# Performance work log

Measured on AMD Instinct MI355X. Metric: run time of the kernel, lower is better.

Reference implementation:

```python
import jax, jax.numpy as jnp
import numpy as np

D_STATE = 16
D_CONV = 4


def _ln_cf(x, w, b, eps=1e-6):
    # channels_first LayerNorm over dim 1 of (B,C,H,W)
    u = x.mean(1, keepdims=True)
    s = ((x - u) ** 2).mean(1, keepdims=True)
    return w[:, None, None] * ((x - u) / jnp.sqrt(s + eps)) + b[:, None, None]


def _ln_last(x, w, b, eps=1e-5):
    u = x.mean(-1, keepdims=True)
    s = ((x - u) ** 2).mean(-1, keepdims=True)
    return (x - u) / jnp.sqrt(s + eps) * w + b


def _mamba(xn, Win, convw, convb, Wx, Wdt, bdt, Alog, Dp):
    # xn: (B, L, d_model); returns (B, L, d_inner) (out_proj is Identity in this module)
    B, L, _ = xn.shape
    di = Win.shape[0] // 2
    xz = xn @ Win.T                                   # (B,L,2*di), in_proj bias=False
    xc, z = xz[..., :di], xz[..., di:]
    # causal depthwise conv1d along L (pad left d_conv-1, slice == torch pad+trim)
    xt = jnp.pad(xc.transpose(0, 2, 1), ((0, 0), (0, 0), (D_CONV - 1, 0)))
    xt = jax.lax.conv_general_dilated(xt, convw[:, None, :], (1,), 'VALID',
                                      dimension_numbers=('NCH', 'OIH', 'NCH'),
                                      feature_group_count=di)
    xs = jax.nn.silu(xt + convb[None, :, None]).transpose(0, 2, 1)  # (B,L,di)
    dtr = Wdt.shape[1]
    x_dbl = xs @ Wx.T                                 # (B,L,dtr+2*ds)
    dt = x_dbl[..., :dtr]
    Bm = x_dbl[..., dtr:dtr + D_STATE]                # (B,L,ds)
    Cm = x_dbl[..., dtr + D_STATE:]                   # (B,L,ds)
    delta = jax.nn.softplus(dt @ Wdt.T + bdt)         # (B,L,di)
    A = -jnp.exp(Alog)                                # (di,ds)
    dA = jnp.exp(delta[..., None] * A)                # (B,L,di,ds)
    dBx = delta[..., None] * Bm[:, :, None, :] * xs[..., None]

    def step(h, ab):
        a, b2 = ab
        h = a * h + b2
        return h, h

    h0 = jnp.zeros((B, di, D_STATE), xn.dtype)
    _, hs = jax.lax.scan(step, h0, (dA.transpose(1, 0, 2, 3), dBx.transpose(1, 0, 2, 3)))
    y = jnp.einsum('lbds,bls->bld', hs, Cm) + xs * Dp
    return y * jax.nn.silu(z)


def _dwconv2d(u, k, dil):
    c = k.shape[0]
    return jax.lax.conv_general_dilated(u, k[:, None], (1, 1),
                                        [(dil, dil), (dil, dil)],
                                        rhs_dilation=(dil, dil),
                                        dimension_numbers=('NCHW', 'OIHW', 'NCHW'),
                                        feature_group_count=c)


def _block(x, gamma1, gamma2, ln1_w, ln1_b, mn_w, mn_b,
           f_Win, f_convw, f_convb, f_Wx, f_Wdt, f_bdt, f_Alog, f_D,
           b_Win, b_convw, b_convb, b_Wx, b_Wdt, b_bdt, b_Alog, b_D,
           Wout, msff_win, msff_dw1, msff_dw2, msff_dw3, msff_wout):
    B, C, H, W = x.shape
    L = H * W
    # --- BiPixelMambaLayer branch ---
    x1 = _ln_cf(x, ln1_w, ln1_b)                       # norm1 (channels_first)
    xf = x1.reshape(B, C, L).transpose(0, 2, 1)        # (B,L,C)
    xn = _ln_last(xf, mn_w, mn_b)                      # inner nn.LayerNorm (eps=1e-5)
    yf = _mamba(xn, f_Win, f_convw, f_convb, f_Wx, f_Wdt, f_bdt, f_Alog, f_D)
    yb = _mamba(xn[:, ::-1], b_Win, b_convw, b_convb, b_Wx, b_Wdt, b_bdt, b_Alog, b_D)
    yo = (yf + yb[:, ::-1]) @ Wout.T                   # shared out_proj (bias=False)
    x = x + gamma1[:, None, None] * (yo.transpose(0, 2, 1).reshape(B, C, H, W) + x1)
    # --- MSFF branch (norm1 reused) ---
    inp = x
    xm = _ln_cf(x, ln1_w, ln1_b)
    h = jnp.einsum('oc,bchw->bohw', msff_win, xm)      # project_in (1x1x1 conv, depth=1)
    hid = msff_dw1.shape[0]
    h1 = _dwconv2d(h[:, :hid], msff_dw1, 1)            # Conv3d 3x3x3 w/ depth=1 == 2D center slice
    h2 = _dwconv2d(h[:, hid:2 * hid], msff_dw2, 2)
    h3 = _dwconv2d(h[:, 2 * hid:], msff_dw3, 3)
    g = jax.nn.gelu(h1, approximate=False) * h2 * h3
    xm = jnp.einsum('oc,bchw->bohw', msff_wout, g)     # project_out
    return inp + gamma2[:, None, None] * xm


def setup_inputs() -> dict:
    key = jax.random.key(0)
    ks = jax.random.split(key, 40)
    dim, di, dtr, ds, hid, Bn, H, W = 96, 192, 6, 16, 192, 2, 64, 64
    r = lambda i, shape, s=0.05: jax.random.normal(ks[i], shape, jnp.float32) * s
    inp = {
        'x': r(0, (Bn, dim, H, W), 1.0),
        'gamma1': r(1, (dim,), 0.1), 'gamma2': r(2, (dim,), 0.1),
        'ln1_w': 1.0 + r(3, (dim,), 0.1), 'ln1_b': r(4, (dim,), 0.1),
        'mn_w': 1.0 + r(5, (dim,), 0.1), 'mn_b': r(6, (dim,), 0.1),
    }
    i = 7
    for p in ('f_', 'b_'):
        inp[p + 'Win'] = r(i, (2 * di, dim)); i += 1
        inp[p + 'convw'] = r(i, (di, D_CONV), 0.2); i += 1
        inp[p + 'convb'] = r(i, (di,), 0.1); i += 1
        inp[p + 'Wx'] = r(i, (dtr + 2 * ds, di)); i += 1
        inp[p + 'Wdt'] = r(i, (di, dtr), 0.1); i += 1
        inp[p + 'bdt'] = r(i, (di,), 0.1); i += 1
        inp[p + 'Alog'] = jax.random.uniform(ks[i], (di, ds), jnp.float32, 0.0, 2.5); i += 1
        inp[p + 'D'] = r(i, (di,), 0.5); i += 1
    inp['Wout'] = r(i, (dim, di)); i += 1
    inp['msff_win'] = r(i, (3 * hid, dim)); i += 1
    inp['msff_dw1'] = r(i, (hid, 3, 3), 0.2); i += 1
    inp['msff_dw2'] = r(i, (hid, 3, 3), 0.2); i += 1
    inp['msff_dw3'] = r(i, (hid, 3, 3), 0.2); i += 1
    inp['msff_wout'] = r(i, (dim, hid)); i += 1
    return inp


def reference(x, gamma1, gamma2, ln1_w, ln1_b, mn_w, mn_b,
              f_Win, f_convw, f_convb, f_Wx, f_Wdt, f_bdt, f_Alog, f_D,
              b_Win, b_convw, b_convb, b_Wx, b_Wdt, b_bdt, b_Alog, b_D,
              Wout, msff_win, msff_dw1, msff_dw2, msff_dw3, msff_wout):
    return _block(x, gamma1, gamma2, ln1_w, ln1_b, mn_w, mn_b,
                  f_Win, f_convw, f_convb, f_Wx, f_Wdt, f_bdt, f_Alog, f_D,
                  b_Win, b_convw, b_convb, b_Wx, b_Wdt, b_bdt, b_Alog, b_D,
                  Wout, msff_win, msff_dw1, msff_dw2, msff_dw3, msff_wout)
```

## Files before the change

### kernel.cpp

```cpp
#include <hip/hip_runtime.h>
#include <hip/hip_bf16.h>
#include <math.h>

typedef __hip_bfloat16 bf16;
typedef _Float16 f16;
typedef f16  f16x8  __attribute__((ext_vector_type(8)));
typedef short short8 __attribute__((ext_vector_type(8)));
typedef float floatx4 __attribute__((ext_vector_type(4)));

#define L_SEQ 4096
#define BATCH 2
#define DIM   96
#define DI    192
#define DS    16
#define HID   192
#define NPOS  (BATCH * L_SEQ)
#define NCH   512
#define CHUNK 8
#define NREC  (2 * BATCH * DI)
#define LDBL  40
#define LOG2E 1.44269504088896f
#define TP    32

__device__ __forceinline__ float silu_f(float x) { return x / (1.f + __expf(-x)); }
__device__ __forceinline__ float softplus_f(float x) {
    return fmaxf(x, 0.f) + __logf(1.f + __expf(-fabsf(x)));
}
__device__ __forceinline__ float b2f(bf16 v) { return __bfloat162float(v); }

__global__ void k_cast_w(const float* __restrict__ fWin, const float* __restrict__ bWin,
                         const float* __restrict__ fWx,  const float* __restrict__ bWx,
                         const float* __restrict__ Wout, const float* __restrict__ mwin,
                         const float* __restrict__ mwout, bf16* __restrict__ arena) {
    int i = blockIdx.x * blockDim.x + threadIdx.x;
    if (i >= 180480) return;
    float v;
    if (i < 36864)        v = fWin[i];
    else if (i < 73728)   v = bWin[i - 36864];
    else if (i < 81024)   v = fWx[i - 73728];
    else if (i < 88320)   v = bWx[i - 81024];
    else if (i < 106752)  v = Wout[i - 88320];
    else if (i < 162048)  v = mwin[i - 106752];
    else                  v = mwout[i - 162048];
    arena[i] = __float2bfloat16(v);
}

__global__ void k_ln12_t(const float* __restrict__ x,
                         const float* __restrict__ ln1w, const float* __restrict__ ln1b,
                         const float* __restrict__ mnw,  const float* __restrict__ mnb,
                         float* __restrict__ X1, bf16* __restrict__ XNbf) {
    __shared__ float xt[DIM][TP + 1];
    __shared__ float rs[8][TP], rss[8][TP];
    __shared__ float uu[TP], rr[TP];
    int p0 = blockIdx.x * TP;
    int b = p0 >> 12, l0 = p0 & (L_SEQ - 1);
    int t = threadIdx.x;
    int tg = t >> 5, li = t & 31;

    for (int idx = t; idx < DIM * TP; idx += 256) {
        int c = idx >> 5, q = idx & 31;
        xt[c][q] = x[((size_t)(b * DIM + c)) * L_SEQ + l0 + q];
    }
    __syncthreads();
    {
        float s = 0.f, ss = 0.f;
        for (int c = tg; c < DIM; c += 8) { float v = xt[c][li]; s += v; ss += v * v; }
        rs[tg][li] = s; rss[tg][li] = ss;
    }
    __syncthreads();
    if (t < TP) {
        float s = 0.f, ss = 0.f;
#pragma unroll
        for (int g = 0; g < 8; g++) { s += rs[g][t]; ss += rss[g][t]; }
        float u = s / DIM;
        uu[t] = u; rr[t] = rsqrtf(ss / DIM - u * u + 1e-6f);
    }
    __syncthreads();
    {
        float u = uu[li], r = rr[li];
        float s2 = 0.f, ss2 = 0.f;
        for (int c = tg; c < DIM; c += 8) {
            float tv = ln1w[c] * (xt[c][li] - u) * r + ln1b[c];
            X1[((size_t)(b * DIM + c)) * L_SEQ + l0 + li] = tv;
            xt[c][li] = tv;
            s2 += tv; ss2 += tv * tv;
        }
        rs[tg][li] = s2; rss[tg][li] = ss2;
    }
    __syncthreads();
    if (t < TP) {
        float s = 0.f, ss = 0.f;
#pragma unroll
        for (int g = 0; g < 8; g++) { s += rs[g][t]; ss += rss[g][t]; }
        float u = s / DIM;
        uu[t] = u; rr[t] = rsqrtf(ss / DIM - u * u + 1e-5f);
    }
    __syncthreads();
    for (int idx = t; idx < DIM * TP; idx += 256) {
        int q = idx / DIM, c = idx % DIM;
        XNbf[(size_t)(p0 + q) * DIM + c] =
            __float2bfloat16((xt[c][q] - uu[q]) * rr[q] * mnw[c] + mnb[c]);
    }
}

__global__ void mfma_nt_dir(const bf16* __restrict__ A0, const bf16* __restrict__ A1,
                            const bf16* __restrict__ W0, const bf16* __restrict__ W1,
                            void* __restrict__ C0, void* __restrict__ C1,
                            int M, int N, int K, int ldc, int pad6, int obf) {
    int z = blockIdx.z;
    const bf16* A = z ? A1 : A0;
    const bf16* W = z ? W1 : W0;
    void* C = z ? C1 : C0;
    int wave = threadIdx.x >> 6, lane = threadIdx.x & 63;
    int m0 = blockIdx.x * 64 + wave * 16;
    int n0 = blockIdx.y * 64;
    int lm = lane & 15, quad = lane >> 4;
    const short* Ap = (const short*)A + (size_t)(m0 + lm) * K + quad * 8;
    const short* Wp = (const short*)W;
    floatx4 acc[4];
#pragma unroll
    for (int t = 0; t < 4; t++) acc[t] = (floatx4){0.f, 0.f, 0.f, 0.f};
    for (int k0 = 0; k0 < K; k0 += 32) {
        short8 a = *(const short8*)(Ap + k0);
#pragma unroll
        for (int t = 0; t < 4; t++) {
            int n = n0 + t * 16 + lm;
            short8 b = (n < N) ? *(const short8*)(Wp + (size_t)n * K + k0 + quad * 8)
                               : (short8){0,0,0,0,0,0,0,0};
            acc[t] = __builtin_amdgcn_mfma_f32_16x16x32_bf16(a, b, acc[t], 0, 0, 0);
        }
    }
#pragma unroll
    for (int t = 0; t < 4; t++) {
        int n = n0 + t * 16 + lm;
        if (n < N) {
            int nn = (pad6 && n >= 6) ? n + 2 : n;
#pragma unroll
            for (int r = 0; r < 4; r++) {
                int m = m0 + quad * 4 + r;
                if (obf) ((bf16*)C)[(size_t)m * ldc + nn] = __float2bfloat16(acc[t][r]);
                else     ((float*)C)[(size_t)m * ldc + nn] = acc[t][r];
            }
        }
    }
}

__global__ void mfma_nt(const bf16* __restrict__ A, const bf16* __restrict__ W,
                        bf16* __restrict__ C, int M, int N, int K, int ldc) {
    int wave = threadIdx.x >> 6, lane = threadIdx.x & 63;
    int m0 = blockIdx.x * 64 + wave * 16;
    int n0 = blockIdx.y * 64;
    int lm = lane & 15, quad = lane >> 4;
    const short* Ap = (const short*)A + (size_t)(m0 + lm) * K + quad * 8;
    const short* Wp = (const short*)W;
    floatx4 acc[4];
#pragma unroll
    for (int t = 0; t < 4; t++) acc[t] = (floatx4){0.f, 0.f, 0.f, 0.f};
    for (int k0 = 0; k0 < K; k0 += 32) {
        short8 a = *(const short8*)(Ap + k0);
#pragma unroll
        for (int t = 0; t < 4; t++) {
            int n = n0 + t * 16 + lm;
            short8 b = (n < N) ? *(const short8*)(Wp + (size_t)n * K + k0 + quad * 8)
                               : (short8){0,0,0,0,0,0,0,0};
            acc[t] = __builtin_amdgcn_mfma_f32_16x16x32_bf16(a, b, acc[t], 0, 0, 0);
        }
    }
#pragma unroll
    for (int t = 0; t < 4; t++) {
        int n = n0 + t * 16 + lm;
        if (n < N) {
#pragma unroll
            for (int r = 0; r < 4; r++) {
                int m = m0 + quad * 4 + r;
                C[(size_t)m * ldc + n] = __float2bfloat16(acc[t][r]);
            }
        }
    }
}

__global__ void mfma_out(const bf16* __restrict__ Y1, const bf16* __restrict__ Y2,
                         const bf16* __restrict__ W, float* __restrict__ C,
                         int M, int N, int K, int ldc) {
    int wave = threadIdx.x >> 6, lane = threadIdx.x & 63;
    int m0 = blockIdx.x * 64 + wave * 16;
    int n0 = blockIdx.y * 64;
    int lm = lane & 15, quad = lane >> 4;
    const short* A1p = (const short*)Y1 + (size_t)(m0 + lm) * K + quad * 8;
    const short* A2p = (const short*)Y2 + (size_t)(m0 + lm) * K + quad * 8;
    const short* Wp  = (const short*)W;
    floatx4 acc[4];
#pragma unroll
    for (int t = 0; t < 4; t++) acc[t] = (floatx4){0.f, 0.f, 0.f, 0.f};
    for (int k0 = 0; k0 < K; k0 += 32) {
        short8 a1 = *(const short8*)(A1p + k0);
        short8 a2 = *(const short8*)(A2p + k0);
#pragma unroll
        for (int t = 0; t < 4; t++) {
            int n = n0 + t * 16 + lm;
            short8 b = (n < N) ? *(const short8*)(Wp + (size_t)n * K + k0 + quad * 8)
                               : (short8){0,0,0,0,0,0,0,0};
            acc[t] = __builtin_amdgcn_mfma_f32_16x16x32_bf16(a1, b, acc[t], 0, 0, 0);
            acc[t] = __builtin_amdgcn_mfma_f32_16x16x32_bf16(a2, b, acc[t], 0, 0, 0);
        }
    }
#pragma unroll
    for (int t = 0; t < 4; t++) {
        int n = n0 + t * 16 + lm;
        if (n < N) {
#pragma unroll
            for (int r = 0; r < 4; r++) {
                int m = m0 + quad * 4 + r;
                C[(size_t)m * ldc + n] = acc[t][r];
            }
        }
    }
}

__global__ void mfma_msffout(const bf16* __restrict__ A, const bf16* __restrict__ Bm,
                             const float* __restrict__ XMID, const float* __restrict__ gamma2,
                             float* __restrict__ out, int M, int K) {
    int wave = threadIdx.x >> 6, lane = threadIdx.x & 63;
    int m0 = blockIdx.x * 64 + wave * 16;
    int n0 = blockIdx.y * 64;
    int lm = lane & 15, quad = lane >> 4;
    int am = m0 + lm;
    bool aval = am < M;
    const short* Ap = (const short*)A + (size_t)am * K + quad * 8;
    const short* Bp = (const short*)Bm;
    floatx4 acc[4];
#pragma unroll
    for (int t = 0; t < 4; t++) acc[t] = (floatx4){0.f, 0.f, 0.f, 0.f};
    for (int k0 = 0; k0 < K; k0 += 32) {
        short8 a = aval ? *(const short8*)(Ap + k0) : (short8){0,0,0,0,0,0,0,0};
#pragma unroll
        for (int t = 0; t < 4; t++) {
            int n = n0 + t * 16 + lm;
            short8 b = *(const short8*)(Bp + (size_t)n * K + k0 + quad * 8);
            acc[t] = __builtin_amdgcn_mfma_f32_16x16x32_bf16(a, b, acc[t], 0, 0, 0);
        }
    }
#pragma unroll
    for (int t = 0; t < 4; t++) {
        int n = n0 + t * 16 + lm;
        int b = n >> 12, l = n & (L_SEQ - 1);
#pragma unroll
        for (int r = 0; r < 4; r++) {
            int m = m0 + quad * 4 + r;
            if (m < M) {
                size_t idx = ((size_t)(b * M + m)) * L_SEQ + l;
                out[idx] = XMID[idx] + gamma2[m] * acc[t][r];
            }
        }
    }
}

__global__ void k_conv(const bf16* __restrict__ XZF, const bf16* __restrict__ XZB,
                       const float* __restrict__ fw, const float* __restrict__ fb,
                       const float* __restrict__ bw, const float* __restrict__ bb,
                       bf16* __restrict__ XSF, bf16* __restrict__ XSB) {
    int dirb = blockIdx.y;
    int i = blockIdx.x * blockDim.x + threadIdx.x;
    int d = i % DI;
    int p = i / DI;
    int b = p >> 12, l = p & (L_SEQ - 1);
    const bf16* XZ = dirb ? XZB : XZF;
    const float* cw = dirb ? bw : fw;
    float acc = (dirb ? bb : fb)[d];
    if (!dirb) {
#pragma unroll
        for (int k = 0; k < 4; k++) {
            int ls = l - 3 + k;
            if (ls >= 0) acc += cw[d * 4 + k] * b2f(XZ[((size_t)(b * L_SEQ + ls)) * 384 + d]);
        }
    } else {
#pragma unroll
        for (int k = 0; k < 4; k++) {
            int ls = l + 3 - k;
            if (ls < L_SEQ) acc += cw[d * 4 + k] * b2f(XZ[((size_t)(b * L_SEQ + ls)) * 384 + d]);
        }
    }
    (dirb ? XSB : XSF)[(size_t)p * DI + d] = __float2bfloat16(silu_f(acc));
}

__global__ void k_scan_p1(const float* __restrict__ DBLF, const float* __restrict__ DBLB,
                          const bf16* __restrict__ XSF,  const bf16* __restrict__ XSB,
                          const float* __restrict__ fWdt, const float* __restrict__ fbdt,
                          const float* __restrict__ bWdt, const float* __restrict__ bbdt,
                          const float* __restrict__ fAlog, const float* __restrict__ bAlog,
                          f16* __restrict__ P, f16* __restrict__ Q) {
    int t = blockIdx.x * blockDim.x + threadIdx.x;
    int d = t % DI;
    int g = t / DI;
    int chunk = g & (NCH - 1);
    int dirb = g >> 9;
    int b = dirb & 1, dir = dirb >> 1;

    const float* DBL = dir ? DBLB : DBLF;
    const bf16*  XS  = dir ? XSB  : XSF;
    const float* al  = (dir ? bAlog : fAlog) + d * DS;
    const float* wdt = (dir ? bWdt : fWdt) + d * 6;
    float bdtv = (dir ? bbdt : fbdt)[d];

    float wd[6];
#pragma unroll
    for (int r = 0; r < 6; r++) wd[r] = wdt[r];
    float A2[16], h[16];
#pragma unroll
    for (int s = 0; s < 16; s++) { A2[s] = -__expf(al[s]) * LOG2E; h[s] = 0.f; }

    int l = dir ? (L_SEQ - 1 - chunk * CHUNK) : chunk * CHUNK;
    int stp = dir ? -1 : 1;
    float sumdel = 0.f;

    for (int i = 0; i < CHUNK; i++) {
        size_t p = (size_t)b * L_SEQ + l;
        const float* row = DBL + p * LDBL;
        float dtv = bdtv;
#pragma unroll
        for (int r = 0; r < 6; r++) dtv += row[r] * wd[r];
        float del = softplus_f(dtv);
        float xs  = b2f(XS[p * DI + d]);
        const float4* bm = (const float4*)(row + 8);
        float4 B0 = bm[0], B1 = bm[1], B2 = bm[2], B3 = bm[3];
        float Bm[16] = {B0.x,B0.y,B0.z,B0.w, B1.x,B1.y,B1.z,B1.w,
                        B2.x,B2.y,B2.z,B2.w, B3.x,B3.y,B3.z,B3.w};
        float dx = del * xs;
        sumdel += del;
#pragma unroll
        for (int s = 0; s < 16; s++) {
            float dA = exp2f(del * A2[s]);
            h[s] = dA * h[s] + dx * Bm[s];
        }
        l += stp;
    }
    size_t idx = ((size_t)g * DI + d) * 16;
    f16x8 q0, q1, p0, p1;
#pragma unroll
    for (int j = 0; j < 8; j++) {
        q0[j] = (f16)h[j];
        q1[j] = (f16)h[8 + j];
        p0[j] = (f16)exp2f(A2[j] * sumdel);
        p1[j] = (f16)exp2f(A2[8 + j] * sumdel);
    }
    *(f16x8*)(Q + idx)     = q0;
    *(f16x8*)(Q + idx + 8) = q1;
    *(f16x8*)(P + idx)     = p0;
    *(f16x8*)(P + idx + 8) = p1;
}

__global__ void k_scan_p2(const f16* __restrict__ P, f16* __restrict__ Q) {
    int u = blockIdx.x * blockDim.x + threadIdx.x;
    int s = u & 15;
    int dd = (u >> 4) % DI;
    int dirb = u / (DI * 16);
    float run = 0.f;
#pragma unroll 8
    for (int c = 0; c < NCH; c++) {
        size_t i = (((size_t)(dirb * NCH + c)) * DI + dd) * 16 + s;
        float tmp = (float)Q[i];
        Q[i] = (f16)run;
        run = (float)P[i] * run + tmp;
    }
}

__global__ void k_scan_p3(const float* __restrict__ DBLF, const float* __restrict__ DBLB,
                          const bf16* __restrict__ XSF,  const bf16* __restrict__ XSB,
                          const bf16* __restrict__ XZF,  const bf16* __restrict__ XZB,
                          const float* __restrict__ fWdt, const float* __restrict__ fbdt,
                          const float* __restrict__ bWdt, const float* __restrict__ bbdt,
                          const float* __restrict__ fAlog, const float* __restrict__ bAlog,
                          const float* __restrict__ fD,    const float* __restrict__ bD,
                          const f16* __restrict__ Q,
                          bf16* __restrict__ YSF, bf16* __restrict__ YSB) {
    int t = blockIdx.x * blockDim.x + threadIdx.x;
    int d = t % DI;
    int g = t / DI;
    int chunk = g & (NCH - 1);
    int dirb = g >> 9;
    int b = dirb & 1, dir = dirb >> 1;

    const float* DBL = dir ? DBLB : DBLF;
    const bf16*  XS  = dir ? XSB  : XSF;
    const bf16*  XZ  = dir ? XZB  : XZF;
    const float* al  = (dir ? bAlog : fAlog) + d * DS;
    const float* wdt = (dir ? bWdt : fWdt) + d * 6;
    float bdtv = (dir ? bbdt : fbdt)[d];
    float Dp = dir ? bD[d] : fD[d];
    bf16* Y = dir ? YSB : YSF;

    float wd[6];
#pragma unroll
    for (int r = 0; r < 6; r++) wd[r] = wdt[r];
    float A2[16], h[16];
#pragma unroll
    for (int s = 0; s < 16; s++) A2[s] = -__expf(al[s]) * LOG2E;
    size_t idx = ((size_t)g * DI + d) * 16;
    f16x8 q0 = *(const f16x8*)(Q + idx);
    f16x8 q1 = *(const f16x8*)(Q + idx + 8);
#pragma unroll
    for (int j = 0; j < 8; j++) { h[j] = (float)q0[j]; h[8 + j] = (float)q1[j]; }

    int l = dir ? (L_SEQ - 1 - chunk * CHUNK) : chunk * CHUNK;
    int stp = dir ? -1 : 1;

    for (int i = 0; i < CHUNK; i++) {
        size_t p = (size_t)b * L_SEQ + l;
        const float* row = DBL + p * LDBL;
        float dtv = bdtv;
#pragma unroll
        for (int r = 0; r < 6; r++) dtv += row[r] * wd[r];
        float del = softplus_f(dtv);
        float xs  = b2f(XS[p * DI + d]);
        float z   = b2f(XZ[p * 384 + 192 + d]);
        const float4* bm = (const float4*)(row + 8);
        float4 B0 = bm[0], B1 = bm[1], B2 = bm[2], B3 = bm[3];
        float4 C0 = bm[4], C1 = bm[5], C2 = bm[6], C3 = bm[7];
        float Bm[16] = {B0.x,B0.y,B0.z,B0.w, B1.x,B1.y,B1.z,B1.w,
                        B2.x,B2.y,B2.z,B2.w, B3.x,B3.y,B3.z,B3.w};
        float Cm[16] = {C0.x,C0.y,C0.z,C0.w, C1.x,C1.y,C1.z,C1.w,
                        C2.x,C2.y,C2.z,C2.w, C3.x,C3.y,C3.z,C3.w};
        float dx = del * xs;
        float pr = 0.f;
#pragma unroll
        for (int s = 0; s < 16; s++) {
            float dA = exp2f(del * A2[s]);
            h[s] = dA * h[s] + dx * Bm[s];
            pr += h[s] * Cm[s];
        }
        Y[p * DI + d] = __float2bfloat16((pr + xs * Dp) * silu_f(z));
        l += stp;
    }
}

__global__ void k_mid_t(const float* __restrict__ x, const float* __restrict__ YO,
                        const float* __restrict__ X1,
                        const float* __restrict__ gamma1,
                        const float* __restrict__ ln1w, const float* __restrict__ ln1b,
                        float* __restrict__ XMID, bf16* __restrict__ XM2cl) {
    __shared__ float vt[DIM][TP + 1];
    __shared__ float yt[DIM][TP + 1];
    __shared__ float rs[8][TP], rss[8][TP];
    __shared__ float uu[TP], rr[TP];
    int p0 = blockIdx.x * TP;
    int b = p0 >> 12, l0 = p0 & (L_SEQ - 1);
    int t = threadIdx.x;
    int tg = t >> 5, li = t & 31;

    for (int idx = t; idx < DIM * TP; idx += 256) {
        int q = idx / DIM, c = idx % DIM;
        yt[c][q] = YO[(size_t)(p0 + q) * DIM + c];
    }
    __syncthreads();
    {
        float s = 0.f, ss = 0.f;
        for (int c = tg; c < DIM; c += 8) {
            size_t gi = ((size_t)(b * DIM + c)) * L_SEQ + l0 + li;
            float v = x[gi] + gamma1[c] * (yt[c][li] + X1[gi]);
            XMID[gi] = v;
            vt[c][li] = v;
            s += v; ss += v * v;
        }
        rs[tg][li] = s; rss[tg][li] = ss;
    }
    __syncthreads();
    if (t < TP) {
        float s = 0.f, ss = 0.f;
#pragma unroll
        for (int g = 0; g < 8; g++) { s += rs[g][t]; ss += rss[g][t]; }
        float u = s / DIM;
        uu[t] = u; rr[t] = rsqrtf(ss / DIM - u * u + 1e-6f);
    }
    __syncthreads();
    for (int idx = t; idx < DIM * TP; idx += 256) {
        int q = idx / DIM, c = idx % DIM;
        XM2cl[(size_t)(p0 + q) * DIM + c] =
            __float2bfloat16(ln1w[c] * (vt[c][q] - uu[q]) * rr[q] + ln1b[c]);
    }
}

__global__ void k_msff(const bf16* __restrict__ H,
                       const float* __restrict__ dw1, const float* __restrict__ dw2,
                       const float* __restrict__ dw3, bf16* __restrict__ G) {
    int i = blockIdx.x * blockDim.x + threadIdx.x;
    int c = i % HID;
    int p = i / HID;
    int b = p >> 12, l = p & (L_SEQ - 1);
    int y = l >> 6, xc = l & 63;
    float a1 = 0.f, a2 = 0.f, a3 = 0.f;
#pragma unroll
    for (int ky = 0; ky < 3; ky++) {
#pragma unroll
        for (int kx = 0; kx < 3; kx++) {
            float w1 = dw1[(c * 3 + ky) * 3 + kx];
            float w2 = dw2[(c * 3 + ky) * 3 + kx];
            float w3 = dw3[(c * 3 + ky) * 3 + kx];
            int y1 = y + (ky - 1), x1 = xc + (kx - 1);
            if (y1 >= 0 && y1 < 64 && x1 >= 0 && x1 < 64)
                a1 += w1 * b2f(H[((size_t)(b * L_SEQ + y1 * 64 + x1)) * 576 + c]);
            int y2 = y + (ky - 1) * 2, x2 = xc + (kx - 1) * 2;
            if (y2 >= 0 && y2 < 64 && x2 >= 0 && x2 < 64)
                a2 += w2 * b2f(H[((size_t)(b * L_SEQ + y2 * 64 + x2)) * 576 + 192 + c]);
            int y3 = y + (ky - 1) * 3, x3 = xc + (kx - 1) * 3;
            if (y3 >= 0 && y3 < 64 && x3 >= 0 && x3 < 64)
                a3 += w3 * b2f(H[((size_t)(b * L_SEQ + y3 * 64 + x3)) * 576 + 384 + c]);
        }
    }
    float ge = 0.5f * a1 * (1.f + erff(a1 * 0.70710678118f));
    G[(size_t)p * HID + c] = __float2bfloat16(ge * a2 * a3);
}

extern "C" void kernel_launch(void* const* d_in, const int* in_sizes, int n_in,
                              void* d_out, int out_size, void* d_ws, size_t ws_size,
                              hipStream_t stream) {
    const float* x      = (const float*)d_in[0];
    const float* gamma1 = (const float*)d_in[1];
    const float* gamma2 = (const float*)d_in[2];
    const float* ln1w   = (const float*)d_in[3];
    const float* ln1b   = (const float*)d_in[4];
    const float* mnw    = (const float*)d_in[5];
    const float* mnb    = (const float*)d_in[6];
    const float* fWin   = (const float*)d_in[7];
    const float* fconvw = (const float*)d_in[8];
    const float* fconvb = (const float*)d_in[9];
    const float* fWx    = (const float*)d_in[10];
    const float* fWdt   = (const float*)d_in[11];
    const float* fbdt   = (const float*)d_in[12];
    const float* fAlog  = (const float*)d_in[13];
    const float* fD     = (const float*)d_in[14];
    const float* bWin   = (const float*)d_in[15];
    const float* bconvw = (const float*)d_in[16];
    const float* bconvb = (const float*)d_in[17];
    const float* bWx    = (const float*)d_in[18];
    const float* bWdt   = (const float*)d_in[19];
    const float* bbdt   = (const float*)d_in[20];
    const float* bAlog  = (const float*)d_in[21];
    const float* bD     = (const float*)d_in[22];
    const float* Wout   = (const float*)d_in[23];
    const float* mwin   = (const float*)d_in[24];
    const float* mdw1   = (const float*)d_in[25];
    const float* mdw2   = (const float*)d_in[26];
    const float* mdw3   = (const float*)d_in[27];
    const float* mwout  = (const float*)d_in[28];
    float* out = (float*)d_out;

    float* ws = (float*)d_ws;
    float* R0    = ws;
    float* X1    = ws + 786432;
    float* XZFr  = ws + 1572864;
    float* XZBr  = ws + 3145728;
    float* XSr   = ws + 4718592;
    float* DBLF  = ws + 6291456;
    float* DBLB  = ws + 6619136;
    float* YSr   = ws + 6946816;
    float* Qr    = ws + 10092544;
    bf16*  WAR   = (bf16*)(ws + 13238272);

    bf16*  XNbf  = (bf16*)R0;
    float* YO    = R0;
    bf16*  XZF   = (bf16*)XZFr;
    bf16*  XZB   = (bf16*)XZBr;
    bf16*  XSF   = (bf16*)XSr;
    bf16*  XSB   = XSF + 1572864;
    f16*   Qh    = (f16*)Qr;
    f16*   Ph    = (f16*)YSr;
    bf16*  YSFbf = (bf16*)YSr;
    bf16*  YSBbf = YSFbf + 1572864;
    float* XMID  = Qr;
    bf16*  XM2cl = (bf16*)(Qr + 786432);
    bf16*  Hcl   = (bf16*)XZFr;
    bf16*  Gcl   = (bf16*)YSr;

    const bf16* fWinB  = WAR;
    const bf16* bWinB  = WAR + 36864;
    const bf16* fWxB   = WAR + 73728;
    const bf16* bWxB   = WAR + 81024;
    const bf16* WoutB  = WAR + 88320;
    const bf16* mwinB  = WAR + 106752;
    const bf16* mwoutB = WAR + 162048;

    k_cast_w<<<705, 256, 0, stream>>>(fWin, bWin, fWx, bWx, Wout, mwin, mwout, WAR);
    k_ln12_t<<<NPOS / TP, 256, 0, stream>>>(x, ln1w, ln1b, mnw, mnb, X1, XNbf);
    mfma_nt_dir<<<dim3(128, 6, 2), 256, 0, stream>>>(XNbf, XNbf, fWinB, bWinB,
                                                     XZF, XZB, NPOS, 384, DIM, 384, 0, 1);
    k_conv<<<dim3(NPOS * DI / 256, 2), 256, 0, stream>>>(XZF, XZB, fconvw, fconvb,
                                                         bconvw, bconvb, XSF, XSB);
    mfma_nt_dir<<<dim3(128, 1, 2), 256, 0, stream>>>(XSF, XSB, fWxB, bWxB,
                                                     DBLF, DBLB, NPOS, 38, DI, LDBL, 1, 0);
    k_scan_p1<<<NREC * NCH / 256, 256, 0, stream>>>(DBLF, DBLB, XSF, XSB,
                                                    fWdt, fbdt, bWdt, bbdt,
                                                    fAlog, bAlog, Ph, Qh);
    k_scan_p2<<<NREC * 16 / 256, 256, 0, stream>>>(Ph, Qh);
    k_scan_p3<<<NREC * NCH / 256, 256, 0, stream>>>(DBLF, DBLB, XSF, XSB, XZF, XZB,
                                                    fWdt, fbdt, bWdt, bbdt,
                                                    fAlog, bAlog, fD, bD, Qh,
                                                    YSFbf, YSBbf);
    mfma_out<<<dim3(128, 2), 256, 0, stream>>>(YSFbf, YSBbf, WoutB, YO, NPOS, DIM, DI, DIM);
    k_mid_t<<<NPOS / TP, 256, 0, stream>>>(x, YO, X1, gamma1, ln1w, ln1b, XMID, XM2cl);
    mfma_nt<<<dim3(128, 9), 256, 0, stream>>>(XM2cl, mwinB, Hcl, NPOS, 576, DIM, 576);
    k_msff<<<NPOS * HID / 256, 256, 0, stream>>>(Hcl, mdw1, mdw2, mdw3, Gcl);
    mfma_msffout<<<dim3(2, 128), 256, 0, stream>>>(mwoutB, Gcl, XMID, gamma2, out, DIM, HID);
}
```

Measured before the change: 316.1 us.

## Vectorize conv and MSFF kernels, precompute scan tables, halve scan chunk size

```diff
diff --git a/kernel.cpp b/kernel.cpp
--- a/kernel.cpp
+++ b/kernel.cpp
@@ -6,6 +6,7 @@
 typedef _Float16 f16;
 typedef f16  f16x8  __attribute__((ext_vector_type(8)));
 typedef short short8 __attribute__((ext_vector_type(8)));
+typedef unsigned short ushort8 __attribute__((ext_vector_type(8)));
 typedef float floatx4 __attribute__((ext_vector_type(4)));
 
 #define L_SEQ 4096
@@ -15,8 +16,8 @@
 #define DS    16
 #define HID   192
 #define NPOS  (BATCH * L_SEQ)
-#define NCH   512
-#define CHUNK 8
+#define NCH   1024
+#define CHUNK 4
 #define NREC  (2 * BATCH * DI)
 #define LDBL  40
 #define LOG2E 1.44269504088896f
@@ -27,22 +28,42 @@
     return fmaxf(x, 0.f) + __logf(1.f + __expf(-fabsf(x)));
 }
 __device__ __forceinline__ float b2f(bf16 v) { return __bfloat162float(v); }
-
-__global__ void k_cast_w(const float* __restrict__ fWin, const float* __restrict__ bWin,
-                         const float* __restrict__ fWx,  const float* __restrict__ bWx,
-                         const float* __restrict__ Wout, const float* __restrict__ mwin,
-                         const float* __restrict__ mwout, bf16* __restrict__ arena) {
+__device__ __forceinline__ float us2f(unsigned short u) {
+    union { unsigned int i; float f; } cv; cv.i = ((unsigned int)u) << 16; return cv.f;
+}
+
+__global__ void k_prep(const float* __restrict__ fWin, const float* __restrict__ bWin,
+                       const float* __restrict__ fWx,  const float* __restrict__ bWx,
+                       const float* __restrict__ Wout, const float* __restrict__ mwin,
+                       const float* __restrict__ mwout,
+                       const float* __restrict__ fAlog, const float* __restrict__ bAlog,
+                       const float* __restrict__ mdw1, const float* __restrict__ mdw2,
+                       const float* __restrict__ mdw3,
+                       bf16* __restrict__ war, float* __restrict__ a2tab,
+                       float* __restrict__ mdwt) {
     int i = blockIdx.x * blockDim.x + threadIdx.x;
-    if (i >= 180480) return;
-    float v;
-    if (i < 36864)        v = fWin[i];
-    else if (i < 73728)   v = bWin[i - 36864];
-    else if (i < 81024)   v = fWx[i - 73728];
-    else if (i < 88320)   v = bWx[i - 81024];
-    else if (i < 106752)  v = Wout[i - 88320];
-    else if (i < 162048)  v = mwin[i - 106752];
-    else                  v = mwout[i - 162048];
-    arena[i] = __float2bfloat16(v);
+    if (i < 180480) {
+        float v;
+        if (i < 36864)        v = fWin[i];
+        else if (i < 73728)   v = bWin[i - 36864];
+        else if (i < 81024)   v = fWx[i - 73728];
+        else if (i < 88320)   v = bWx[i - 81024];
+        else if (i < 106752)  v = Wout[i - 88320];
+        else if (i < 162048)  v = mwin[i - 106752];
+        else                  v = mwout[i - 162048];
+        war[i] = __float2bfloat16(v);
+    } else if (i < 186624) {
+        int j = i - 180480;
+        int dir = j / 3072, rem = j % 3072;
+        const float* al = dir ? bAlog : fAlog;
+        a2tab[j] = -__expf(al[rem]) * LOG2E;
+    } else if (i < 191808) {
+        int j = i - 186624;
+        int cv = j / 1728, rem = j % 1728;
+        int tap = rem / 192, c = rem % 192;
+        const float* src = (cv == 0) ? mdw1 : (cv == 1) ? mdw2 : mdw3;
+        mdwt[j] = src[c * 9 + tap];
+    }
 }
 
 __global__ void k_ln12_t(const float* __restrict__ x,
@@ -255,64 +276,85 @@
     }
 }
 
-__global__ void k_conv(const bf16* __restrict__ XZF, const bf16* __restrict__ XZB,
-                       const float* __restrict__ fw, const float* __restrict__ fb,
-                       const float* __restrict__ bw, const float* __restrict__ bb,
-                       bf16* __restrict__ XSF, bf16* __restrict__ XSB) {
+__global__ void k_conv_v(const bf16* __restrict__ XZF, const bf16* __restrict__ XZB,
+                         const float* __restrict__ fw, const float* __restrict__ fb,
+                         const float* __restrict__ bw, const float* __restrict__ bb,
+                         bf16* __restrict__ XSF, bf16* __restrict__ XSB) {
     int dirb = blockIdx.y;
     int i = blockIdx.x * blockDim.x + threadIdx.x;
-    int d = i % DI;
-    int p = i / DI;
+    int dg = i % 24;
+    int p = i / 24;
     int b = p >> 12, l = p & (L_SEQ - 1);
+    int d0 = dg * 8;
     const bf16* XZ = dirb ? XZB : XZF;
     const float* cw = dirb ? bw : fw;
-    float acc = (dirb ? bb : fb)[d];
-    if (!dirb) {
-#pragma unroll
-        for (int k = 0; k < 4; k++) {
-            int ls = l - 3 + k;
-            if (ls >= 0) acc += cw[d * 4 + k] * b2f(XZ[((size_t)(b * L_SEQ + ls)) * 384 + d]);
-        }
-    } else {
-#pragma unroll
-        for (int k = 0; k < 4; k++) {
-            int ls = l + 3 - k;
-            if (ls < L_SEQ) acc += cw[d * 4 + k] * b2f(XZ[((size_t)(b * L_SEQ + ls)) * 384 + d]);
-        }
-    }
-    (dirb ? XSB : XSF)[(size_t)p * DI + d] = __float2bfloat16(silu_f(acc));
+    const float* cb = dirb ? bb : fb;
+
+    float4 w[8];
+#pragma unroll
+    for (int j = 0; j < 8; j++) w[j] = *(const float4*)(cw + (d0 + j) * 4);
+    float acc[8];
+#pragma unroll
+    for (int j = 0; j < 8; j++) acc[j] = cb[d0 + j];
+
+#pragma unroll
+    for (int k = 0; k < 4; k++) {
+        int ls = dirb ? (l + 3 - k) : (l - 3 + k);
+        if (ls >= 0 && ls < L_SEQ) {
+            ushort8 xv = *(const ushort8*)((const unsigned short*)XZ +
+                           ((size_t)(b * L_SEQ + ls)) * 384 + d0);
+#pragma unroll
+            for (int j = 0; j < 8; j++) {
+                float wk = (k == 0) ? w[j].x : (k == 1) ? w[j].y : (k == 2) ? w[j].z : w[j].w;
+                acc[j] += wk * us2f(xv[j]);
+            }
+        }
+    }
+    ushort8 ov;
+#pragma unroll
+    for (int j = 0; j < 8; j++) {
+        bf16 t = __float2bfloat16(silu_f(acc[j]));
+        ov[j] = *(unsigned short*)&t;
+    }
+    *(ushort8*)((unsigned short*)(dirb ? XSB : XSF) + (size_t)p * DI + d0) = ov;
 }
 
 __global__ void k_scan_p1(const float* __restrict__ DBLF, const float* __restrict__ DBLB,
                           const bf16* __restrict__ XSF,  const bf16* __restrict__ XSB,
                           const float* __restrict__ fWdt, const float* __restrict__ fbdt,
                           const float* __restrict__ bWdt, const float* __restrict__ bbdt,
-                          const float* __restrict__ fAlog, const float* __restrict__ bAlog,
+                          const float* __restrict__ a2tab,
                           f16* __restrict__ P, f16* __restrict__ Q) {
     int t = blockIdx.x * blockDim.x + threadIdx.x;
     int d = t % DI;
     int g = t / DI;
     int chunk = g & (NCH - 1);
-    int dirb = g >> 9;
+    int dirb = g >> 10;
     int b = dirb & 1, dir = dirb >> 1;
 
     const float* DBL = dir ? DBLB : DBLF;
     const bf16*  XS  = dir ? XSB  : XSF;
-    const float* al  = (dir ? bAlog : fAlog) + d * DS;
     const float* wdt = (dir ? bWdt : fWdt) + d * 6;
     float bdtv = (dir ? bbdt : fbdt)[d];
 
     float wd[6];
 #pragma unroll
     for (int r = 0; r < 6; r++) wd[r] = wdt[r];
+    const float* a2p = a2tab + (dir * DI + d) * 16;
     float A2[16], h[16];
 #pragma unroll
-    for (int s = 0; s < 16; s++) { A2[s] = -__expf(al[s]) * LOG2E; h[s] = 0.f; }
+    for (int v = 0; v < 4; v++) {
+        float4 a2v = *(const float4*)(a2p + 4 * v);
+        A2[4*v] = a2v.x; A2[4*v+1] = a2v.y; A2[4*v+2] = a2v.z; A2[4*v+3] = a2v.w;
+    }
+#pragma unroll
+    for (int s = 0; s < 16; s++) h[s] = 0.f;
 
     int l = dir ? (L_SEQ - 1 - chunk * CHUNK) : chunk * CHUNK;
     int stp = dir ? -1 : 1;
     float sumdel = 0.f;
 
+#pragma unroll
     for (int i = 0; i < CHUNK; i++) {
         size_t p = (size_t)b * L_SEQ + l;
         const float* row = DBL + p * LDBL;
@@ -369,7 +411,7 @@
                           const bf16* __restrict__ XZF,  const bf16* __restrict__ XZB,
                           const float* __restrict__ fWdt, const float* __restrict__ fbdt,
                           const float* __restrict__ bWdt, const float* __restrict__ bbdt,
-                          const float* __restrict__ fAlog, const float* __restrict__ bAlog,
+                          const float* __restrict__ a2tab,
                           const float* __restrict__ fD,    const float* __restrict__ bD,
                           const f16* __restrict__ Q,
                           bf16* __restrict__ YSF, bf16* __restrict__ YSB) {
@@ -377,13 +419,12 @@
     int d = t % DI;
     int g = t / DI;
     int chunk = g & (NCH - 1);
-    int dirb = g >> 9;
+    int dirb = g >> 10;
     int b = dirb & 1, dir = dirb >> 1;
 
     const float* DBL = dir ? DBLB : DBLF;
     const bf16*  XS  = dir ? XSB  : XSF;
     const bf16*  XZ  = dir ? XZB  : XZF;
-    const float* al  = (dir ? bAlog : fAlog) + d * DS;
     const float* wdt = (dir ? bWdt : fWdt) + d * 6;
     float bdtv = (dir ? bbdt : fbdt)[d];
     float Dp = dir ? bD[d] : fD[d];
@@ -392,9 +433,13 @@
     float wd[6];
 #pragma unroll
     for (int r = 0; r < 6; r++) wd[r] = wdt[r];
+    const float* a2p = a2tab + (dir * DI + d) * 16;
     float A2[16], h[16];
 #pragma unroll
-    for (int s = 0; s < 16; s++) A2[s] = -__expf(al[s]) * LOG2E;
+    for (int v = 0; v < 4; v++) {
+        float4 a2v = *(const float4*)(a2p + 4 * v);
+        A2[4*v] = a2v.x; A2[4*v+1] = a2v.y; A2[4*v+2] = a2v.z; A2[4*v+3] = a2v.w;
+    }
     size_t idx = ((size_t)g * DI + d) * 16;
     f16x8 q0 = *(const f16x8*)(Q + idx);
     f16x8 q1 = *(const f16x8*)(Q + idx + 8);
@@ -404,6 +449,7 @@
     int l = dir ? (L_SEQ - 1 - chunk * CHUNK) : chunk * CHUNK;
     int stp = dir ? -1 : 1;
 
+#pragma unroll
     for (int i = 0; i < CHUNK; i++) {
         size_t p = (size_t)b * L_SEQ + l;
         const float* row = DBL + p * LDBL;
@@ -479,35 +525,68 @@
     }
 }
 
-__global__ void k_msff(const bf16* __restrict__ H,
-                       const float* __restrict__ dw1, const float* __restrict__ dw2,
-                       const float* __restrict__ dw3, bf16* __restrict__ G) {
+__global__ void k_msff_v(const bf16* __restrict__ H, const float* __restrict__ mdwt,
+                         bf16* __restrict__ G) {
     int i = blockIdx.x * blockDim.x + threadIdx.x;
-    int c = i % HID;
-    int p = i / HID;
+    int cg = i % 24;
+    int p = i / 24;
+    int c0 = cg * 8;
     int b = p >> 12, l = p & (L_SEQ - 1);
     int y = l >> 6, xc = l & 63;
-    float a1 = 0.f, a2 = 0.f, a3 = 0.f;
+    float a1[8] = {}, a2[8] = {}, a3[8] = {};
+    const unsigned short* Hu = (const unsigned short*)H;
+
 #pragma unroll
     for (int ky = 0; ky < 3; ky++) {
 #pragma unroll
         for (int kx = 0; kx < 3; kx++) {
-            float w1 = dw1[(c * 3 + ky) * 3 + kx];
-            float w2 = dw2[(c * 3 + ky) * 3 + kx];
-            float w3 = dw3[(c * 3 + ky) * 3 + kx];
-            int y1 = y + (ky - 1), x1 = xc + (kx - 1);
-            if (y1 >= 0 && y1 < 64 && x1 >= 0 && x1 < 64)
-                a1 += w1 * b2f(H[((size_t)(b * L_SEQ + y1 * 64 + x1)) * 576 + c]);
-            int y2 = y + (ky - 1) * 2, x2 = xc + (kx - 1) * 2;
-            if (y2 >= 0 && y2 < 64 && x2 >= 0 && x2 < 64)
-                a2 += w2 * b2f(H[((size_t)(b * L_SEQ + y2 * 64 + x2)) * 576 + 192 + c]);
-            int y3 = y + (ky - 1) * 3, x3 = xc + (kx - 1) * 3;
-            if (y3 >= 0 && y3 < 64 && x3 >= 0 && x3 < 64)
-                a3 += w3 * b2f(H[((size_t)(b * L_SEQ + y3 * 64 + x3)) * 576 + 384 + c]);
-        }
-    }
-    float ge = 0.5f * a1 * (1.f + erff(a1 * 0.70710678118f));
-    G[(size_t)p * HID + c] = __float2bfloat16(ge * a2 * a3);
+            int tap = ky * 3 + kx;
+            {
+                int y1 = y + (ky - 1), x1 = xc + (kx - 1);
+                if (y1 >= 0 && y1 < 64 && x1 >= 0 && x1 < 64) {
+                    float4 w0 = *(const float4*)(mdwt + tap * 192 + c0);
+                    float4 w1 = *(const float4*)(mdwt + tap * 192 + c0 + 4);
+                    ushort8 hv = *(const ushort8*)(Hu +
+                        ((size_t)(b * L_SEQ + y1 * 64 + x1)) * 576 + c0);
+                    float wv[8] = {w0.x,w0.y,w0.z,w0.w, w1.x,w1.y,w1.z,w1.w};
+#pragma unroll
+                    for (int j = 0; j < 8; j++) a1[j] += wv[j] * us2f(hv[j]);
+                }
+            }
+            {
+                int y2 = y + (ky - 1) * 2, x2 = xc + (kx - 1) * 2;
+                if (y2 >= 0 && y2 < 64 && x2 >= 0 && x2 < 64) {
+                    float4 w0 = *(const float4*)(mdwt + (9 + tap) * 192 + c0);
+                    float4 w1 = *(const float4*)(mdwt + (9 + tap) * 192 + c0 + 4);
+                    ushort8 hv = *(const ushort8*)(Hu +
+                        ((size_t)(b * L_SEQ + y2 * 64 + x2)) * 576 + 192 + c0);
+                    float wv[8] = {w0.x,w0.y,w0.z,w0.w, w1.x,w1.y,w1.z,w1.w};
+#pragma unroll
+                    for (int j = 0; j < 8; j++) a2[j] += wv[j] * us2f(hv[j]);
+                }
+            }
+            {
+                int y3 = y + (ky - 1) * 3, x3 = xc + (kx - 1) * 3;
+                if (y3 >= 0 && y3 < 64 && x3 >= 0 && x3 < 64) {
+                    float4 w0 = *(const float4*)(mdwt + (18 + tap) * 192 + c0);
+                    float4 w1 = *(const float4*)(mdwt + (18 + tap) * 192 + c0 + 4);
+                    ushort8 hv = *(const ushort8*)(Hu +
+                        ((size_t)(b * L_SEQ + y3 * 64 + x3)) * 576 + 384 + c0);
+                    float wv[8] = {w0.x,w0.y,w0.z,w0.w, w1.x,w1.y,w1.z,w1.w};
+#pragma unroll
+                    for (int j = 0; j < 8; j++) a3[j] += wv[j] * us2f(hv[j]);
+                }
+            }
+        }
+    }
+    ushort8 ov;
+#pragma unroll
+    for (int j = 0; j < 8; j++) {
+        float ge = 0.5f * a1[j] * (1.f + erff(a1[j] * 0.70710678118f));
+        bf16 t = __float2bfloat16(ge * a2[j] * a3[j]);
+        ov[j] = *(unsigned short*)&t;
+    }
+    *(ushort8*)((unsigned short*)G + (size_t)p * HID + c0) = ov;
 }
 
 extern "C" void kernel_launch(void* const* d_in, const int* in_sizes, int n_in,
@@ -545,31 +624,26 @@
     float* out = (float*)d_out;
 
     float* ws = (float*)d_ws;
-    float* R0    = ws;
-    float* X1    = ws + 786432;
-    float* XZFr  = ws + 1572864;
-    float* XZBr  = ws + 3145728;
-    float* XSr   = ws + 4718592;
-    float* DBLF  = ws + 6291456;
-    float* DBLB  = ws + 6619136;
-    float* YSr   = ws + 6946816;
-    float* Qr    = ws + 10092544;
-    bf16*  WAR   = (bf16*)(ws + 13238272);
-
-    bf16*  XNbf  = (bf16*)R0;
-    float* YO    = R0;
-    bf16*  XZF   = (bf16*)XZFr;
-    bf16*  XZB   = (bf16*)XZBr;
-    bf16*  XSF   = (bf16*)XSr;
-    bf16*  XSB   = XSF + 1572864;
-    f16*   Qh    = (f16*)Qr;
-    f16*   Ph    = (f16*)YSr;
-    bf16*  YSFbf = (bf16*)YSr;
-    bf16*  YSBbf = YSFbf + 1572864;
-    float* XMID  = Qr;
-    bf16*  XM2cl = (bf16*)(Qr + 786432);
-    bf16*  Hcl   = (bf16*)XZFr;
-    bf16*  Gcl   = (bf16*)YSr;
+    float* X1    = ws;
+    bf16*  XNbf  = (bf16*)(ws + 786432);
+    bf16*  XZF   = (bf16*)(ws + 1179648);
+    bf16*  XZB   = (bf16*)(ws + 2752512);
+    bf16*  XSF   = (bf16*)(ws + 4325376);
+    bf16*  XSB   = (bf16*)(ws + 5111808);
+    float* DBLF  = ws + 5898240;
+    float* DBLB  = ws + 6225920;
+    f16*   Ph    = (f16*)(ws + 6553600);
+    f16*   Qh    = (f16*)(ws + 12845056);
+    bf16*  YSFbf = (bf16*)(ws + 19136512);
+    bf16*  YSBbf = (bf16*)(ws + 19922944);
+    float* YO    = ws + 20709376;
+    float* XMID  = ws + 21495808;
+    bf16*  XM2cl = (bf16*)(ws + 22282240);
+    bf16*  Hcl   = (bf16*)(ws + 22675456);
+    bf16*  Gcl   = (bf16*)(ws + 25034752);
+    bf16*  WAR   = (bf16*)(ws + 25821184);
+    float* A2tab = ws + 25911424;
+    float* MDWT  = ws + 25917568;
 
     const bf16* fWinB  = WAR;
     const bf16* bWinB  = WAR + 36864;
@@ -579,25 +653,27 @@
     const bf16* mwinB  = WAR + 106752;
     const bf16* mwoutB = WAR + 162048;
 
-    k_cast_w<<<705, 256, 0, stream>>>(fWin, bWin, fWx, bWx, Wout, mwin, mwout, WAR);
+    k_prep<<<750, 256, 0, stream>>>(fWin, bWin, fWx, bWx, Wout, mwin, mwout,
+                                    fAlog, bAlog, mdw1, mdw2, mdw3,
+                                    WAR, A2tab, MDWT);
     k_ln12_t<<<NPOS / TP, 256, 0, stream>>>(x, ln1w, ln1b, mnw, mnb, X1, XNbf);
     mfma_nt_dir<<<dim3(128, 6, 2), 256, 0, stream>>>(XNbf, XNbf, fWinB, bWinB,
                                                      XZF, XZB, NPOS, 384, DIM, 384, 0, 1);
-    k_conv<<<dim3(NPOS * DI / 256, 2), 256, 0, stream>>>(XZF, XZB, fconvw, fconvb,
-                                                         bconvw, bconvb, XSF, XSB);
+    k_conv_v<<<dim3(NPOS * 24 / 256, 2), 256, 0, stream>>>(XZF, XZB, fconvw, fconvb,
+                                                           bconvw, bconvb, XSF, XSB);
     mfma_nt_dir<<<dim3(128, 1, 2), 256, 0, stream>>>(XSF, XSB, fWxB, bWxB,
                                                      DBLF, DBLB, NPOS, 38, DI, LDBL, 1, 0);
     k_scan_p1<<<NREC * NCH / 256, 256, 0, stream>>>(DBLF, DBLB, XSF, XSB,
                                                     fWdt, fbdt, bWdt, bbdt,
-                                                    fAlog, bAlog, Ph, Qh);
+                                                    A2tab, Ph, Qh);
     k_scan_p2<<<NREC * 16 / 256, 256, 0, stream>>>(Ph, Qh);
     k_scan_p3<<<NREC * NCH / 256, 256, 0, stream>>>(DBLF, DBLB, XSF, XSB, XZF, XZB,
                                                     fWdt, fbdt, bWdt, bbdt,
-                                                    fAlog, bAlog, fD, bD, Qh,
+                                                    A2tab, fD, bD, Qh,
                                                     YSFbf, YSBbf);
     mfma_out<<<dim3(128, 2), 256, 0, stream>>>(YSFbf, YSBbf, WoutB, YO, NPOS, DIM, DI, DIM);
     k_mid_t<<<NPOS / TP, 256, 0, stream>>>(x, YO, X1, gamma1, ln1w, ln1b, XMID, XM2cl);
     mfma_nt<<<dim3(128, 9), 256, 0, stream>>>(XM2cl, mwinB, Hcl, NPOS, 576, DIM, 576);
-    k_msff<<<NPOS * HID / 256, 256, 0, stream>>>(Hcl, mdw1, mdw2, mdw3, Gcl);
+    k_msff_v<<<NPOS * 24 / 256, 256, 0, stream>>>(Hcl, MDWT, Gcl);
     mfma_msffout<<<dim3(2, 128), 256, 0, stream>>>(mwoutB, Gcl, XMID, gamma2, out, DIM, HID);
 }
```

Result: no change. 315.8 us (-0.1%).
